# Kernel tuning notes

Measured on AMD Instinct MI355X. Metric: run time of the kernel, lower is better.

The kernel has to match this reference:

```python
import jax, jax.numpy as jnp
import numpy as np

EPS = 1e-6
MAX_ITER = 3

def skew(w):
    z = jnp.zeros_like(w[:, 0])
    return jnp.stack([
        jnp.stack([z, -w[:, 2], w[:, 1]], -1),
        jnp.stack([w[:, 2], z, -w[:, 0]], -1),
        jnp.stack([-w[:, 1], w[:, 0], z], -1)], -2)

def twist2mat(w):
    # Rodrigues formula, w: [B,3] -> R: [B,3,3]
    theta = jnp.linalg.norm(w, axis=-1, keepdims=True) + 1e-12
    axis = w / theta
    Km = skew(axis)
    th = theta[..., None]
    I = jnp.eye(3, dtype=w.dtype)
    return I + jnp.sin(th) * Km + (1.0 - jnp.cos(th)) * (Km @ Km)

def sobel_gradient(img, normalize=True):
    # replicate-pad + 3x3 Sobel, img: [B,C,H,W]
    p = jnp.pad(img, ((0, 0), (0, 0), (1, 1), (1, 1)), mode='edge')
    tl = p[..., :-2, :-2]; tc = p[..., :-2, 1:-1]; tr = p[..., :-2, 2:]
    ml = p[..., 1:-1, :-2]; mr = p[..., 1:-1, 2:]
    bl = p[..., 2:, :-2]; bc = p[..., 2:, 1:-1]; br = p[..., 2:, 2:]
    dx = (tr - tl) + 2.0 * (mr - ml) + (br - bl)
    dy = (bl - tl) + 2.0 * (bc - tc) + (br - tr)
    if normalize:
        mag = jnp.sqrt(dx * dx + dy * dy + 1e-8)
        dx, dy = dx / mag, dy / mag
    return dx, dy

def _bilinear_one(F, u, v):
    # F: [C,H,W]; u,v: [H,W] pixel coords; border padding (grid_sample-like)
    C, H, W = F.shape
    u = jnp.clip(u, 0.0, W - 1.0)
    v = jnp.clip(v, 0.0, H - 1.0)
    x0 = jnp.floor(u); y0 = jnp.floor(v)
    wx = u - x0; wy = v - y0
    x0i = x0.astype(jnp.int32); y0i = y0.astype(jnp.int32)
    x1i = jnp.minimum(x0i + 1, W - 1); y1i = jnp.minimum(y0i + 1, H - 1)
    g = lambda yi, xi: F[:, yi, xi]  # advanced-index gather -> [C,H,W]
    return (g(y0i, x0i) * (1 - wx) * (1 - wy) + g(y0i, x1i) * wx * (1 - wy)
            + g(y1i, x0i) * (1 - wx) * wy + g(y1i, x1i) * wx * wy)

def warp_features(F, u, v):
    # F: [B,C,H,W]; u,v: [B,1,H,W]
    return jax.vmap(_bilinear_one)(F, u[:, 0], v[:, 0])

def generate_xy_grid(B, H, W, K):
    fx, fy, cx, cy = [K[:, i].reshape(B, 1, 1, 1) for i in range(4)]
    uu, vv = jnp.meshgrid(jnp.arange(W, dtype=K.dtype), jnp.arange(H, dtype=K.dtype))
    px = (uu[None, None] - cx) / fx
    py = (vv[None, None] - cy) / fy
    return px, py  # [B,1,H,W] each

def batch_warp_inverse_depth(px, py, invD0, R, t, K):
    B, _, H, W = px.shape
    xy1 = jnp.concatenate([px, py, jnp.ones_like(px)], 1).reshape(B, 3, -1)
    warped = R @ xy1 + t[:, :, None] * invD0.reshape(B, 1, -1)
    x_, y_, s_ = warped[:, 0], warped[:, 1], warped[:, 2]
    fx, fy, cx, cy = [K[:, i].reshape(B, 1) for i in range(4)]
    u_ = (x_ / s_ * fx + cx).reshape(B, 1, H, W)
    v_ = (y_ / s_ * fy + cy).reshape(B, 1, H, W)
    inv_z = invD0 / s_.reshape(B, 1, H, W)
    return u_, v_, inv_z

def check_occ(inv_z_buffer, invD1, u, v, thres=0.1):
    B, _, H, W = invD1.shape
    inv_z_warped = warp_features(invD1, u, v)
    inlier = inv_z_buffer > inv_z_warped - thres
    inview = (u > 0) & (u < W) & (v > 0) & (v < H)
    return ~(inlier & inview)  # [B,1,H,W] bool

def compute_jacobian_warping(invD, K, px, py):
    # linearized at origin (pose=None branch)
    B, _, H, W = invD.shape
    x = px.reshape(B, -1); y = py.reshape(B, -1); d = invD.reshape(B, -1)
    O = jnp.zeros_like(x)
    xy = x * y
    dx_dp = jnp.stack([-xy, 1.0 + x * x, -y, d, O, -d * x], -1)
    dy_dp = jnp.stack([-(1.0 + y * y), xy, x, O, d, -d * y], -1)
    fx = K[:, 0].reshape(B, 1, 1); fy = K[:, 1].reshape(B, 1, 1)
    return dx_dp * fx, dy_dp * fy  # [B,HW,6] each

def lev_mar_H(JtWJ):
    diag = jnp.eye(6, dtype=JtWJ.dtype)
    trace = jnp.trace(JtWJ, axis1=1, axis2=2)
    return JtWJ + (trace * 1e-6)[:, None, None] * diag

def forward(twist0, x0, x1, invD0, invD1, sigma0, sigma1, K):
    B, C, H, W = x0.shape
    N = H * W
    dtype = x0.dtype
    R = twist2mat(twist0[:, :3])
    t = twist0[:, 3:]
    px, py = generate_xy_grid(B, H, W, K)
    # inverse-compositional: template Jacobian precomputed once
    Jf_x, Jf_y = sobel_gradient(x0, normalize=True)
    Jx_p, Jy_p = compute_jacobian_warping(invD0, K, px, py)
    J = (Jf_x.reshape(B, C, N, 1) * Jx_p.reshape(B, 1, N, 6)
         + Jf_y.reshape(B, C, N, 1) * Jy_p.reshape(B, 1, N, 6))  # [B,C,N,6]
    for _ in range(MAX_ITER):
        u_w, v_w, inv_z = batch_warp_inverse_depth(px, py, invD0, R, t, K)
        occ = check_occ(inv_z, invD1, u_w, v_w)
        f_r = warp_features(x1, u_w, v_w)
        sigma_r = warp_features(sigma1, u_w, v_w)
        res = f_r - x0
        sigma = jnp.sqrt(sigma_r * sigma_r + sigma0 * sigma0)
        wres = jnp.where(occ, EPS, res / sigma)  # [B,C,H,W]
        valid = (~occ).reshape(B, 1, N, 1).astype(dtype)
        Jw = (J / sigma.reshape(B, C, N, 1) * valid).reshape(B, C * N, 6)
        r = jnp.where(occ, 0.0, wres).reshape(B, C * N)
        JtWJ = jnp.einsum('bnk,bnl->bkl', Jw, Jw)
        Rhs = jnp.einsum('bnk,bn->bk', Jw, r)[..., None]
        xi = jnp.linalg.solve(lev_mar_H(JtWJ), Rhs)  # [B,6,1]
        d_R = twist2mat(-xi[:, :3, 0])
        d_t = -(d_R @ xi[:, 3:])
        t = (R @ d_t)[:, :, 0] + t
        R = R @ d_R
    return jnp.concatenate([R.reshape(B, 9), t], axis=1)  # [B,12]

def setup_inputs() -> dict:
    key = jax.random.key(0)
    ks = jax.random.split(key, 7)
    B, C, H, W = 8, 16, 240, 320
    twist0 = jax.random.normal(ks[0], (B, 6), jnp.float32) * 0.01
    x0 = jax.random.normal(ks[1], (B, C, H, W), jnp.float32)
    x1 = jax.random.normal(ks[2], (B, C, H, W), jnp.float32)
    invD0 = jax.random.uniform(ks[3], (B, 1, H, W), jnp.float32, 0.1, 1.0)
    invD1 = jax.random.uniform(ks[4], (B, 1, H, W), jnp.float32, 0.1, 1.0)
    sigma0 = jax.random.uniform(ks[5], (B, C, H, W), jnp.float32, 0.1, 1.0)
    sigma1 = jax.random.uniform(ks[6], (B, C, H, W), jnp.float32, 0.1, 1.0)
    Kmat = jnp.tile(jnp.array([[0.8 * W, 0.8 * W, W / 2.0, H / 2.0]], jnp.float32), (B, 1))
    return dict(twist0=twist0, x0=x0, x1=x1, invD0=invD0, invD1=invD1,
                sigma0=sigma0, sigma1=sigma1, K=Kmat)

def reference(twist0, x0, x1, invD0, invD1, sigma0, sigma1, K):
    return forward(twist0, x0, x1, invD0, invD1, sigma0, sigma1, K)
```

## Files before the change

kernel.cpp:

```cpp
#include <hip/hip_runtime.h>
#include <hip/hip_fp16.h>

#define B_ 8
#define C_ 16
#define H_ 240
#define W_ 320
#define N_ (H_*W_)
#define ITER_BLOCKS ((N_/512)*B_)

__device__ __forceinline__ void twist2mat_dev(float w0, float w1, float w2, float R[9]) {
    float th = sqrtf(w0*w0 + w1*w1 + w2*w2) + 1e-12f;
    float ax = w0/th, ay = w1/th, az = w2/th;
    float s = sinf(th), c = cosf(th), ic = 1.0f - c;
    R[0] = 1.0f + ic*(ax*ax - 1.0f);
    R[1] = -s*az + ic*ax*ay;
    R[2] =  s*ay + ic*ax*az;
    R[3] =  s*az + ic*ax*ay;
    R[4] = 1.0f + ic*(ay*ay - 1.0f);
    R[5] = -s*ax + ic*ay*az;
    R[6] = -s*ay + ic*ax*az;
    R[7] =  s*ax + ic*ay*az;
    R[8] = 1.0f + ic*(az*az - 1.0f);
}

__device__ __forceinline__ unsigned pack_h2(float a, float b) {
    __half2 h = __floats2half2_rn(a, b);
    return *reinterpret_cast<unsigned*>(&h);
}
__device__ __forceinline__ float2 unpack_h2(unsigned u) {
    __half2 h = *reinterpret_cast<__half2*>(&u);
    return __half22float2(h);
}

__device__ __forceinline__ void solve_update(const float* __restrict__ ac, float R[9], float t[3]) {
    float M[6][7];
    {
        int idx = 0;
        #pragma unroll
        for (int k = 0; k < 6; k++)
            #pragma unroll
            for (int l = k; l < 6; l++) { M[k][l] = ac[idx]; M[l][k] = ac[idx]; idx++; }
    }
    const float trace = M[0][0]+M[1][1]+M[2][2]+M[3][3]+M[4][4]+M[5][5];
    const float lam = trace * 1e-6f;
    #pragma unroll
    for (int i = 0; i < 6; i++) { M[i][i] += lam; M[i][6] = ac[21+i]; }

    #pragma unroll
    for (int k = 0; k < 6; k++) {
        const float inv = 1.0f / M[k][k];
        #pragma unroll
        for (int i = k+1; i < 6; i++) {
            const float f = M[i][k] * inv;
            #pragma unroll
            for (int j = k; j < 7; j++) M[i][j] -= f * M[k][j];
        }
    }
    float xi[6];
    #pragma unroll
    for (int i = 5; i >= 0; i--) {
        float s = M[i][6];
        #pragma unroll
        for (int j = i+1; j < 6; j++) s -= M[i][j]*xi[j];
        xi[i] = s / M[i][i];
    }

    float dR[9];
    twist2mat_dev(-xi[0], -xi[1], -xi[2], dR);
    const float dt0 = -(dR[0]*xi[3] + dR[1]*xi[4] + dR[2]*xi[5]);
    const float dt1 = -(dR[3]*xi[3] + dR[4]*xi[4] + dR[5]*xi[5]);
    const float dt2 = -(dR[6]*xi[3] + dR[7]*xi[4] + dR[8]*xi[5]);

    const float nt0 = R[0]*dt0 + R[1]*dt1 + R[2]*dt2 + t[0];
    const float nt1 = R[3]*dt0 + R[4]*dt1 + R[5]*dt2 + t[1];
    const float nt2 = R[6]*dt0 + R[7]*dt1 + R[8]*dt2 + t[2];
    float nR[9];
    #pragma unroll
    for (int i = 0; i < 3; i++)
        #pragma unroll
        for (int j = 0; j < 3; j++)
            nR[i*3+j] = R[i*3+0]*dR[0*3+j] + R[i*3+1]*dR[1*3+j] + R[i*3+2]*dR[2*3+j];
    #pragma unroll
    for (int i = 0; i < 9; i++) R[i] = nR[i];
    t[0] = nt0; t[1] = nt1; t[2] = nt2;
}

__device__ __forceinline__ void build_RT(const float* __restrict__ twist0,
                                         const float* __restrict__ accum,
                                         int b, int iters, float R[9], float t[3]) {
    const float* w = twist0 + b*6;
    twist2mat_dev(w[0], w[1], w[2], R);
    t[0] = w[3]; t[1] = w[4]; t[2] = w[5];
    for (int j = 0; j < iters; j++)
        solve_update(accum + (size_t)(j*B_ + b)*27, R, t);
}

__launch_bounds__(256)
__global__ void precompute_kernel(const float* __restrict__ x0, const float* __restrict__ x1,
                                  const float* __restrict__ sigma0, const float* __restrict__ sigma1,
                                  uint4* __restrict__ P0h, uint4* __restrict__ X1S1h,
                                  float* __restrict__ accum, unsigned* __restrict__ counter)
{
    if (blockIdx.x == 0 && blockIdx.y == 0 && blockIdx.z == 0) {
        for (int k = threadIdx.x; k < 3*B_*27; k += 256) accum[k] = 0.0f;
        if (threadIdx.x == 0) *counter = 0u;
    }
    const int b  = blockIdx.z;
    const int cg = blockIdx.y;
    const int base_pix = blockIdx.x * 256;
    const int pix = base_pix + threadIdx.x;
    const int h0 = base_pix / W_;

    __shared__ float lds[4][4][W_];
    __shared__ float auxl[3][4][256];

    const size_t cbase = ((size_t)(b*C_) + cg*4) * N_;

    #pragma unroll
    for (int k = 0; k < 5; k++) {
        const int idx = threadIdx.x + k*256;
        const int ch  = idx / 320;
        const int rem = idx - ch*320;
        const int row = rem / 80;
        const int c4  = rem - row*80;
        const int src_r = min(max(h0 - 1 + row, 0), H_ - 1);
        const float4 v = *reinterpret_cast<const float4*>(
            x0 + cbase + (size_t)ch*N_ + (size_t)src_r*W_ + c4*4);
        *reinterpret_cast<float4*>(&lds[ch][row][c4*4]) = v;
    }
    {
        const int ch = threadIdx.x >> 6;
        const int c4 = threadIdx.x & 63;
        const size_t off = cbase + (size_t)ch*N_ + base_pix + c4*4;
        const float4 v0 = *reinterpret_cast<const float4*>(x1     + off);
        const float4 v1 = *reinterpret_cast<const float4*>(sigma0 + off);
        const float4 v2 = *reinterpret_cast<const float4*>(sigma1 + off);
        *reinterpret_cast<float4*>(&auxl[0][ch][c4*4]) = v0;
        *reinterpret_cast<float4*>(&auxl[1][ch][c4*4]) = v1;
        *reinterpret_cast<float4*>(&auxl[2][ch][c4*4]) = v2;
    }
    __syncthreads();

    const int h = pix / W_;
    const int w = pix - h*W_;
    const int lr = h - (h0 - 1);
    const int wm = max(w-1, 0), wp = min(w+1, W_-1);

    unsigned gq[4], xq[4], qq[4];
    #pragma unroll
    for (int i = 0; i < 4; i++) {
        const float* rT = lds[i][lr-1];
        const float* rM = lds[i][lr];
        const float* rB = lds[i][lr+1];
        const float tl = rT[wm], tc_ = rT[w], tr = rT[wp];
        const float ml = rM[wm], ctr = rM[w], mr = rM[wp];
        const float bl = rB[wm], bc_ = rB[w], br = rB[wp];
        const float dx = tr - tl + 2.0f*(mr - ml) + (br - bl);
        const float dy = bl - tl + 2.0f*(bc_ - tc_) + (br - tr);
        const float mag = sqrtf(dx*dx + dy*dy + 1e-8f);
        const float s0v = auxl[1][i][threadIdx.x];
        gq[i] = pack_h2(dx/mag, dy/mag);
        xq[i] = pack_h2(ctr, s0v*s0v);
        qq[i] = pack_h2(auxl[0][i][threadIdx.x], auxl[2][i][threadIdx.x]);
    }

    uint4 A;  A.x = gq[0];  A.y = xq[0];  A.z = gq[1];  A.w = xq[1];
    uint4 Bw; Bw.x = gq[2]; Bw.y = xq[2]; Bw.z = gq[3]; Bw.w = xq[3];
    uint4 Q;  Q.x = qq[0];  Q.y = qq[1];  Q.z = qq[2];  Q.w = qq[3];
    P0h[((size_t)(b*8 + cg*2  ))*N_ + pix] = A;
    P0h[((size_t)(b*8 + cg*2+1))*N_ + pix] = Bw;
    X1S1h[((size_t)(b*4 + cg))*N_ + pix] = Q;
}

__device__ __forceinline__ void accum_pixel(int pix,
                                            const float Rm[9], const float tv[3],
                                            float fx, float fy, float cx, float cy,
                                            const uint4* __restrict__ P0b,
                                            const uint4* __restrict__ X1S1b,
                                            const float* __restrict__ d0,
                                            const float* __restrict__ dz,
                                            float* __restrict__ acc)
{
    const int h = pix / W_;
    const int w = pix - h*W_;

    const float px = ((float)w - cx) / fx;
    const float py = ((float)h - cy) / fy;
    const float d  = d0[pix];

    const float x_ = Rm[0]*px + Rm[1]*py + Rm[2] + tv[0]*d;
    const float y_ = Rm[3]*px + Rm[4]*py + Rm[5] + tv[1]*d;
    const float s_ = Rm[6]*px + Rm[7]*py + Rm[8] + tv[2]*d;
    const float u = x_/s_*fx + cx;
    const float v = y_/s_*fy + cy;
    const float inv_z = d / s_;

    const float uc = fminf(fmaxf(u, 0.0f), (float)(W_-1));
    const float vc = fminf(fmaxf(v, 0.0f), (float)(H_-1));
    const float x0f = floorf(uc), y0f = floorf(vc);
    const float wx = uc - x0f, wy = vc - y0f;
    const int x0i = (int)x0f, y0i = (int)y0f;
    const int x1i = min(x0i+1, W_-1), y1i = min(y0i+1, H_-1);
    const float w00 = (1.0f-wx)*(1.0f-wy), w01 = wx*(1.0f-wy);
    const float w10 = (1.0f-wx)*wy,        w11 = wx*wy;
    const int i00 = y0i*W_+x0i, i01 = y0i*W_+x1i, i10 = y1i*W_+x0i, i11 = y1i*W_+x1i;

    const float zw = dz[i00]*w00 + dz[i01]*w01 + dz[i10]*w10 + dz[i11]*w11;
    const bool inlier = inv_z > zw - 0.1f;
    const bool inview = (u > 0.0f) && (u < (float)W_) && (v > 0.0f) && (v < (float)H_);
    const bool valid  = inlier && inview;

    if (!valid) return;

    const float xy = px*py;
    const float Av[6] = { -xy*fx, (1.0f+px*px)*fx, -py*fx, d*fx, 0.0f, -d*px*fx };
    const float Bv[6] = { -(1.0f+py*py)*fy, xy*fy, px*fy, 0.0f, d*fy, -d*py*fy };

    float Swxx=0.f, Swxy=0.f, Swyy=0.f, Srx=0.f, Sry=0.f;

#define CH(gword, xword, t00, t01, t10, t11) { \
    const float2 g  = unpack_h2(gword); \
    const float2 xs = unpack_h2(xword); \
    const float2 a00 = unpack_h2(t00), a01 = unpack_h2(t01), \
                 a10 = unpack_h2(t10), a11 = unpack_h2(t11); \
    const float fr = a00.x*w00 + a01.x*w01 + a10.x*w10 + a11.x*w11; \
    const float sr = a00.y*w00 + a01.y*w01 + a10.y*w10 + a11.y*w11; \
    const float inv_s2 = 1.0f/(sr*sr + xs.y); \
    const float res = fr - xs.x; \
    const float gxw = g.x*inv_s2, gyw = g.y*inv_s2; \
    Swxx += g.x*gxw; Swxy += g.x*gyw; Swyy += g.y*gyw; \
    Srx  += res*gxw; Sry  += res*gyw; }

    #pragma unroll
    for (int cgi = 0; cgi < 4; cgi++) {
        const uint4 pA = P0b[(size_t)(cgi*2  )*N_ + pix];
        const uint4 pB = P0b[(size_t)(cgi*2+1)*N_ + pix];
        const uint4* xsb = X1S1b + (size_t)cgi*N_;
        const uint4 q00 = xsb[i00], q01 = xsb[i01], q10 = xsb[i10], q11 = xsb[i11];
        CH(pA.x, pA.y, q00.x, q01.x, q10.x, q11.x)
        CH(pA.z, pA.w, q00.y, q01.y, q10.y, q11.y)
        CH(pB.x, pB.y, q00.z, q01.z, q10.z, q11.z)
        CH(pB.z, pB.w, q00.w, q01.w, q10.w, q11.w)
    }
#undef CH

    int idx = 0;
    #pragma unroll
    for (int k = 0; k < 6; k++) {
        #pragma unroll
        for (int l = k; l < 6; l++) {
            acc[idx++] += Swxx*Av[k]*Av[l] + Swxy*(Av[k]*Bv[l] + Bv[k]*Av[l]) + Swyy*Bv[k]*Bv[l];
        }
    }
    #pragma unroll
    for (int k = 0; k < 6; k++) acc[21+k] += Srx*Av[k] + Sry*Bv[k];
}

__launch_bounds__(256)
__global__ void iter_kernel(const uint4* __restrict__ P0h, const uint4* __restrict__ X1S1h,
                            const float* __restrict__ invD0, const float* __restrict__ invD1,
                            const float* __restrict__ Kmat, const float* __restrict__ twist0,
                            float* __restrict__ accum, unsigned* __restrict__ counter,
                            float* __restrict__ out, int it, int do_final)
{
    const int b = blockIdx.y;
    const int pix0 = blockIdx.x * 512 + threadIdx.x;

    float Rm[9], tv[3];
    build_RT(twist0, accum, b, it, Rm, tv);

    const float fx = Kmat[b*4+0], fy = Kmat[b*4+1], cx = Kmat[b*4+2], cy = Kmat[b*4+3];

    float acc[27];
    #pragma unroll
    for (int j = 0; j < 27; j++) acc[j] = 0.0f;

    const uint4* P0b   = P0h   + (size_t)b*8*N_;
    const uint4* X1S1b = X1S1h + (size_t)b*4*N_;
    const float* d0 = invD0 + b*N_;
    const float* dz = invD1 + b*N_;

    accum_pixel(pix0,       Rm, tv, fx, fy, cx, cy, P0b, X1S1b, d0, dz, acc);
    accum_pixel(pix0 + 256, Rm, tv, fx, fy, cx, cy, P0b, X1S1b, d0, dz, acc);

    const int lane = threadIdx.x & 63;
    const int wave = threadIdx.x >> 6;
    __shared__ float red[4][27];
    #pragma unroll
    for (int j = 0; j < 27; j++) {
        float vv = acc[j];
        vv += __shfl_down(vv, 32);
        vv += __shfl_down(vv, 16);
        vv += __shfl_down(vv, 8);
        vv += __shfl_down(vv, 4);
        vv += __shfl_down(vv, 2);
        vv += __shfl_down(vv, 1);
        if (lane == 0) red[wave][j] = vv;
    }
    __syncthreads();
    if (threadIdx.x < 27) {
        float s = red[0][threadIdx.x] + red[1][threadIdx.x] + red[2][threadIdx.x] + red[3][threadIdx.x];
        atomicAdd(&accum[(size_t)(it*B_ + b)*27 + threadIdx.x], s);
    }

    if (do_final) {
        __shared__ int amlast;
        __syncthreads();
        if (threadIdx.x == 0) {
            __threadfence();
            amlast = (atomicAdd(counter, 1u) == (unsigned)(ITER_BLOCKS - 1)) ? 1 : 0;
        }
        __syncthreads();
        if (amlast && threadIdx.x < B_) {
            const int fb = threadIdx.x;
            float fR[9], ft[3];
            build_RT(twist0, accum, fb, 3, fR, ft);
            float* ob = out + fb*12;
            #pragma unroll
            for (int i = 0; i < 9; i++) ob[i] = fR[i];
            ob[9] = ft[0]; ob[10] = ft[1]; ob[11] = ft[2];
        }
    }
}

extern "C" void kernel_launch(void* const* d_in, const int* in_sizes, int n_in,
                              void* d_out, int out_size, void* d_ws, size_t ws_size,
                              hipStream_t stream) {
    const float* twist0 = (const float*)d_in[0];
    const float* x0     = (const float*)d_in[1];
    const float* x1     = (const float*)d_in[2];
    const float* invD0  = (const float*)d_in[3];
    const float* invD1  = (const float*)d_in[4];
    const float* sigma0 = (const float*)d_in[5];
    const float* sigma1 = (const float*)d_in[6];
    const float* Kmat   = (const float*)d_in[7];
    float* out = (float*)d_out;

    const size_t p0_bytes = (size_t)B_*8*N_*sizeof(uint4);
    const size_t xs_bytes = (size_t)B_*4*N_*sizeof(uint4);

    uint4* P0h   = (uint4*)d_ws;
    uint4* X1S1h = (uint4*)((char*)d_ws + p0_bytes);
    float* accum = (float*)((char*)d_ws + p0_bytes + xs_bytes);
    unsigned* counter = (unsigned*)(accum + 3*B_*27);

    hipLaunchKernelGGL(precompute_kernel, dim3(N_/256, 4, B_), dim3(256), 0, stream,
                       x0, x1, sigma0, sigma1, P0h, X1S1h, accum, counter);

    dim3 grid(N_/512, B_);
    for (int it = 0; it < 3; ++it) {
        hipLaunchKernelGGL(iter_kernel, grid, dim3(256), 0, stream,
                           P0h, X1S1h, invD0, invD1, Kmat, twist0, accum, counter, out,
                           it, (it == 2) ? 1 : 0);
    }
}
```

Measured before the change: 357.8 us.

## Solve pose update once per iteration in last block and halve pixels per thread

Previously every block rebuilt R,t by redoing all prior 6x6 Gauss-Newton solves from the accumulated sums. Now the last block of each iteration, detected with a per-iteration atomic counter, solves once and writes R,t to a workspace buffer that the next launch reads. The initial pose is built in the precompute kernel. The iteration grid also doubles to one pixel per thread with a launch_bounds occupancy hint of 8. This adds an atomic counter and a threadfence per block on every iteration, and the solve now runs serially in one block through shared memory.

```diff
diff --git a/kernel.cpp b/kernel.cpp
--- a/kernel.cpp
+++ b/kernel.cpp
@@ -6,7 +6,7 @@
 #define H_ 240
 #define W_ 320
 #define N_ (H_*W_)
-#define ITER_BLOCKS ((N_/512)*B_)
+#define ITER_BLOCKS ((N_/256)*B_)
 
 __device__ __forceinline__ void twist2mat_dev(float w0, float w1, float w2, float R[9]) {
     float th = sqrtf(w0*w0 + w1*w1 + w2*w2) + 1e-12f;
@@ -32,78 +32,26 @@
     return __half22float2(h);
 }
 
-__device__ __forceinline__ void solve_update(const float* __restrict__ ac, float R[9], float t[3]) {
-    float M[6][7];
-    {
-        int idx = 0;
-        #pragma unroll
-        for (int k = 0; k < 6; k++)
-            #pragma unroll
-            for (int l = k; l < 6; l++) { M[k][l] = ac[idx]; M[l][k] = ac[idx]; idx++; }
-    }
-    const float trace = M[0][0]+M[1][1]+M[2][2]+M[3][3]+M[4][4]+M[5][5];
-    const float lam = trace * 1e-6f;
-    #pragma unroll
-    for (int i = 0; i < 6; i++) { M[i][i] += lam; M[i][6] = ac[21+i]; }
-
-    #pragma unroll
-    for (int k = 0; k < 6; k++) {
-        const float inv = 1.0f / M[k][k];
-        #pragma unroll
-        for (int i = k+1; i < 6; i++) {
-            const float f = M[i][k] * inv;
-            #pragma unroll
-            for (int j = k; j < 7; j++) M[i][j] -= f * M[k][j];
-        }
-    }
-    float xi[6];
-    #pragma unroll
-    for (int i = 5; i >= 0; i--) {
-        float s = M[i][6];
-        #pragma unroll
-        for (int j = i+1; j < 6; j++) s -= M[i][j]*xi[j];
-        xi[i] = s / M[i][i];
-    }
-
-    float dR[9];
-    twist2mat_dev(-xi[0], -xi[1], -xi[2], dR);
-    const float dt0 = -(dR[0]*xi[3] + dR[1]*xi[4] + dR[2]*xi[5]);
-    const float dt1 = -(dR[3]*xi[3] + dR[4]*xi[4] + dR[5]*xi[5]);
-    const float dt2 = -(dR[6]*xi[3] + dR[7]*xi[4] + dR[8]*xi[5]);
-
-    const float nt0 = R[0]*dt0 + R[1]*dt1 + R[2]*dt2 + t[0];
-    const float nt1 = R[3]*dt0 + R[4]*dt1 + R[5]*dt2 + t[1];
-    const float nt2 = R[6]*dt0 + R[7]*dt1 + R[8]*dt2 + t[2];
-    float nR[9];
-    #pragma unroll
-    for (int i = 0; i < 3; i++)
-        #pragma unroll
-        for (int j = 0; j < 3; j++)
-            nR[i*3+j] = R[i*3+0]*dR[0*3+j] + R[i*3+1]*dR[1*3+j] + R[i*3+2]*dR[2*3+j];
-    #pragma unroll
-    for (int i = 0; i < 9; i++) R[i] = nR[i];
-    t[0] = nt0; t[1] = nt1; t[2] = nt2;
-}
-
-__device__ __forceinline__ void build_RT(const float* __restrict__ twist0,
-                                         const float* __restrict__ accum,
-                                         int b, int iters, float R[9], float t[3]) {
-    const float* w = twist0 + b*6;
-    twist2mat_dev(w[0], w[1], w[2], R);
-    t[0] = w[3]; t[1] = w[4]; t[2] = w[5];
-    for (int j = 0; j < iters; j++)
-        solve_update(accum + (size_t)(j*B_ + b)*27, R, t);
-}
-
 __launch_bounds__(256)
 __global__ void precompute_kernel(const float* __restrict__ x0, const float* __restrict__ x1,
                                   const float* __restrict__ sigma0, const float* __restrict__ sigma1,
+                                  const float* __restrict__ twist0,
                                   uint4* __restrict__ P0h, uint4* __restrict__ X1S1h,
-                                  float* __restrict__ accum, unsigned* __restrict__ counter)
+                                  float* __restrict__ accum, unsigned* __restrict__ counters,
+                                  float* __restrict__ RT)
 {
     if (blockIdx.x == 0 && blockIdx.y == 0 && blockIdx.z == 0) {
         for (int k = threadIdx.x; k < 3*B_*27; k += 256) accum[k] = 0.0f;
-        if (threadIdx.x == 0) *counter = 0u;
+        if (threadIdx.x < 3) counters[threadIdx.x] = 0u;
+        if (threadIdx.x < B_) {
+            const float* w = twist0 + threadIdx.x*6;
+            float R[9];
+            twist2mat_dev(w[0], w[1], w[2], R);
+            float* rt = RT + threadIdx.x*12;
+            #pragma unroll
+            for (int i = 0; i < 9; i++) rt[i] = R[i];
+            rt[9] = w[3]; rt[10] = w[4]; rt[11] = w[5];
+        }
     }
     const int b  = blockIdx.z;
     const int cg = blockIdx.y;
@@ -256,18 +204,22 @@
     for (int k = 0; k < 6; k++) acc[21+k] += Srx*Av[k] + Sry*Bv[k];
 }
 
-__launch_bounds__(256)
+__launch_bounds__(256, 8)
 __global__ void iter_kernel(const uint4* __restrict__ P0h, const uint4* __restrict__ X1S1h,
                             const float* __restrict__ invD0, const float* __restrict__ invD1,
-                            const float* __restrict__ Kmat, const float* __restrict__ twist0,
-                            float* __restrict__ accum, unsigned* __restrict__ counter,
-                            float* __restrict__ out, int it, int do_final)
+                            const float* __restrict__ Kmat,
+                            float* __restrict__ RT, float* __restrict__ accum,
+                            unsigned* __restrict__ counters, float* __restrict__ out,
+                            int it, int last)
 {
     const int b = blockIdx.y;
-    const int pix0 = blockIdx.x * 512 + threadIdx.x;
-
+    const int pix = blockIdx.x * 256 + threadIdx.x;
+
+    const float* rt = RT + (size_t)(it*B_ + b)*12;
     float Rm[9], tv[3];
-    build_RT(twist0, accum, b, it, Rm, tv);
+    #pragma unroll
+    for (int i = 0; i < 9; i++) Rm[i] = rt[i];
+    tv[0] = rt[9]; tv[1] = rt[10]; tv[2] = rt[11];
 
     const float fx = Kmat[b*4+0], fy = Kmat[b*4+1], cx = Kmat[b*4+2], cy = Kmat[b*4+3];
 
@@ -280,8 +232,7 @@
     const float* d0 = invD0 + b*N_;
     const float* dz = invD1 + b*N_;
 
-    accum_pixel(pix0,       Rm, tv, fx, fy, cx, cy, P0b, X1S1b, d0, dz, acc);
-    accum_pixel(pix0 + 256, Rm, tv, fx, fy, cx, cy, P0b, X1S1b, d0, dz, acc);
+    accum_pixel(pix, Rm, tv, fx, fy, cx, cy, P0b, X1S1b, d0, dz, acc);
 
     const int lane = threadIdx.x & 63;
     const int wave = threadIdx.x >> 6;
@@ -303,22 +254,73 @@
         atomicAdd(&accum[(size_t)(it*B_ + b)*27 + threadIdx.x], s);
     }
 
-    if (do_final) {
-        __shared__ int amlast;
-        __syncthreads();
-        if (threadIdx.x == 0) {
-            __threadfence();
-            amlast = (atomicAdd(counter, 1u) == (unsigned)(ITER_BLOCKS - 1)) ? 1 : 0;
-        }
-        __syncthreads();
-        if (amlast && threadIdx.x < B_) {
-            const int fb = threadIdx.x;
-            float fR[9], ft[3];
-            build_RT(twist0, accum, fb, 3, fR, ft);
-            float* ob = out + fb*12;
+    __shared__ int amlast;
+    __syncthreads();
+    if (threadIdx.x == 0) {
+        __threadfence();
+        amlast = (atomicAdd(&counters[it], 1u) == (unsigned)(ITER_BLOCKS - 1)) ? 1 : 0;
+    }
+    __syncthreads();
+    if (amlast && threadIdx.x < B_) {
+        const int bb = threadIdx.x;
+        __shared__ float Ms[B_][44];
+        float* M = Ms[bb];
+        const float* ac = accum + (size_t)(it*B_ + bb)*27;
+        {
+            int idx = 0;
+            for (int k = 0; k < 6; k++)
+                for (int l = k; l < 6; l++) { M[k*7+l] = ac[idx]; M[l*7+k] = ac[idx]; idx++; }
+        }
+        const float trace = M[0]+M[8]+M[16]+M[24]+M[32]+M[40];
+        const float lam = trace * 1e-6f;
+        for (int i = 0; i < 6; i++) { M[i*7+i] += lam; M[i*7+6] = ac[21+i]; }
+
+        for (int k = 0; k < 6; k++) {
+            const float inv = 1.0f / M[k*7+k];
+            for (int i = k+1; i < 6; i++) {
+                const float f = M[i*7+k] * inv;
+                for (int j = k; j < 7; j++) M[i*7+j] -= f * M[k*7+j];
+            }
+        }
+        float xi[6];
+        for (int i = 5; i >= 0; i--) {
+            float s = M[i*7+6];
+            for (int j = i+1; j < 6; j++) s -= M[i*7+j]*xi[j];
+            xi[i] = s / M[i*7+i];
+        }
+
+        const float* rtc = RT + (size_t)(it*B_ + bb)*12;
+        float R[9], t[3];
+        #pragma unroll
+        for (int i = 0; i < 9; i++) R[i] = rtc[i];
+        t[0] = rtc[9]; t[1] = rtc[10]; t[2] = rtc[11];
+
+        float dR[9];
+        twist2mat_dev(-xi[0], -xi[1], -xi[2], dR);
+        const float dt0 = -(dR[0]*xi[3] + dR[1]*xi[4] + dR[2]*xi[5]);
+        const float dt1 = -(dR[3]*xi[3] + dR[4]*xi[4] + dR[5]*xi[5]);
+        const float dt2 = -(dR[6]*xi[3] + dR[7]*xi[4] + dR[8]*xi[5]);
+
+        const float nt0 = R[0]*dt0 + R[1]*dt1 + R[2]*dt2 + t[0];
+        const float nt1 = R[3]*dt0 + R[4]*dt1 + R[5]*dt2 + t[1];
+        const float nt2 = R[6]*dt0 + R[7]*dt1 + R[8]*dt2 + t[2];
+        float nR[9];
+        #pragma unroll
+        for (int i = 0; i < 3; i++)
             #pragma unroll
-            for (int i = 0; i < 9; i++) ob[i] = fR[i];
-            ob[9] = ft[0]; ob[10] = ft[1]; ob[11] = ft[2];
+            for (int j = 0; j < 3; j++)
+                nR[i*3+j] = R[i*3+0]*dR[0*3+j] + R[i*3+1]*dR[1*3+j] + R[i*3+2]*dR[2*3+j];
+
+        float* rtn = RT + (size_t)((it+1)*B_ + bb)*12;
+        #pragma unroll
+        for (int i = 0; i < 9; i++) rtn[i] = nR[i];
+        rtn[9] = nt0; rtn[10] = nt1; rtn[11] = nt2;
+
+        if (last) {
+            float* ob = out + bb*12;
+            #pragma unroll
+            for (int i = 0; i < 9; i++) ob[i] = nR[i];
+            ob[9] = nt0; ob[10] = nt1; ob[11] = nt2;
         }
     }
 }
@@ -342,15 +344,16 @@
     uint4* P0h   = (uint4*)d_ws;
     uint4* X1S1h = (uint4*)((char*)d_ws + p0_bytes);
     float* accum = (float*)((char*)d_ws + p0_bytes + xs_bytes);
-    unsigned* counter = (unsigned*)(accum + 3*B_*27);
+    unsigned* counters = (unsigned*)(accum + 3*B_*27);
+    float* RT = (float*)(counters + 8);
 
     hipLaunchKernelGGL(precompute_kernel, dim3(N_/256, 4, B_), dim3(256), 0, stream,
-                       x0, x1, sigma0, sigma1, P0h, X1S1h, accum, counter);
-
-    dim3 grid(N_/512, B_);
+                       x0, x1, sigma0, sigma1, twist0, P0h, X1S1h, accum, counters, RT);
+
+    dim3 grid(N_/256, B_);
     for (int it = 0; it < 3; ++it) {
         hipLaunchKernelGGL(iter_kernel, grid, dim3(256), 0, stream,
-                           P0h, X1S1h, invD0, invD1, Kmat, twist0, accum, counter, out,
+                           P0h, X1S1h, invD0, invD1, Kmat, RT, accum, counters, out,
                            it, (it == 2) ? 1 : 0);
     }
 }
```

Result: slower. 937.9 us (+162.1%).
